# Kernel optimization log

Hardware: AMD Instinct MI355X
Metric: run time of the kernel (lower is better)

The kernel has to match this reference:

```python
import jax, jax.numpy as jnp
import numpy as np

NUM_EMBEDDINGS = 8192
EMBEDDING_DIM = 256
COMMITMENT_COST = 0.25


def setup_inputs() -> dict:
    key = jax.random.key(0)
    k1, k2 = jax.random.split(key)
    z_e = jax.random.normal(k1, (16, 2048, EMBEDDING_DIM), dtype=jnp.float32)
    # nn.Embedding init: uniform(-1/K, 1/K)
    codebook = jax.random.uniform(
        k2, (NUM_EMBEDDINGS, EMBEDDING_DIM), dtype=jnp.float32,
        minval=-1.0 / NUM_EMBEDDINGS, maxval=1.0 / NUM_EMBEDDINGS)
    return {"z_e": z_e, "codebook": codebook}


def _nearest_indices(z_flat, codebook):
    # squared euclidean distances; argmin is identical to argmin of cdist
    # z_flat: [T, D], codebook: [K, D] -> dist2: [T, K]
    x2 = jnp.sum(z_flat * z_flat, axis=-1, keepdims=True)          # [T, 1]
    w2 = jnp.sum(codebook * codebook, axis=-1)                      # [K]
    xw = jnp.einsum('td,kd->tk', z_flat, codebook)                  # [T, K]
    dist2 = x2 - 2.0 * xw + w2
    return jnp.argmin(dist2, axis=1)                                # [T]


def reference(z_e, codebook):
    original_shape = z_e.shape
    z_e_flat = z_e.reshape(-1, EMBEDDING_DIM)
    indices = _nearest_indices(z_e_flat, codebook)
    z_q = codebook[indices].reshape(original_shape)
    # straight-through estimator
    z_q_ste = z_e + jax.lax.stop_gradient(z_q - z_e)
    commitment_loss = jnp.mean((z_e - jax.lax.stop_gradient(z_q_ste)) ** 2)
    codebook_loss = jnp.mean((z_q_ste - jax.lax.stop_gradient(z_e)) ** 2)
    loss = codebook_loss + COMMITMENT_COST * commitment_loss
    # codebook usage: fraction of unique indices (jit-friendly via scatter)
    used = jnp.zeros((NUM_EMBEDDINGS,), dtype=jnp.float32).at[indices].set(1.0)
    usage = jnp.sum(used) / NUM_EMBEDDINGS
    return (z_q_ste, loss, usage)
```

## Files before the change

kernel.cpp:

```cpp
#include <hip/hip_runtime.h>
#include <float.h>

#define T_TOTAL 32768
#define KC      8192
#define DIM     256

#define LOSS_IDX  ((size_t)T_TOTAL * DIM)
#define USAGE_IDX (LOSS_IDX + 1)

typedef short s16x8 __attribute__((ext_vector_type(8)));
typedef float f32x4 __attribute__((ext_vector_type(4)));

#define WS_W2    0
#define WS_FLAGS 32768
#define WS_CBF   65536

__device__ __forceinline__ unsigned short f2bf(float f) {
    unsigned int u = __float_as_uint(f);
    u += 0x7FFFu + ((u >> 16) & 1u);
    return (unsigned short)(u >> 16);
}

__global__ __launch_bounds__(256) void vq_prep(const float* __restrict__ cb,
                                               unsigned short* __restrict__ cbb,
                                               float* __restrict__ w2,
                                               int* __restrict__ flags,
                                               float* __restrict__ out) {
    const int blk = blockIdx.x, tid = threadIdx.x;
    size_t i = (size_t)blk * 2048 + (size_t)tid * 8;
    float4 a = *(const float4*)(cb + i);
    float4 b = *(const float4*)(cb + i + 4);
    uint4 o;
    o.x = (unsigned)f2bf(a.x) | ((unsigned)f2bf(a.y) << 16);
    o.y = (unsigned)f2bf(a.z) | ((unsigned)f2bf(a.w) << 16);
    o.z = (unsigned)f2bf(b.x) | ((unsigned)f2bf(b.y) << 16);
    o.w = (unsigned)f2bf(b.z) | ((unsigned)f2bf(b.w) << 16);
    *(uint4*)(cbb + i) = o;
    float s = a.x * a.x + a.y * a.y + a.z * a.z + a.w * a.w
            + b.x * b.x + b.y * b.y + b.z * b.z + b.w * b.w;
    #pragma unroll
    for (int m = 1; m <= 16; m <<= 1) s += __shfl_xor(s, m);
    if ((tid & 31) == 0) w2[blk * 8 + (tid >> 5)] = s;
    if (blk < 32) flags[blk * 256 + tid] = 0;
    if (blk < 128) {
        int t = blk * 256 + tid;
        *(unsigned long long*)(out + ((size_t)t << 8)) = ~0ULL;
    }
    if (blk == 0 && tid == 0) { out[LOSS_IDX] = 0.0f; out[USAGE_IDX] = 0.0f; }
}

__global__ __launch_bounds__(512, 2) void vq_main(const unsigned short* __restrict__ cbb,
                                                  const float* __restrict__ w2g,
                                                  const float* __restrict__ z_e,
                                                  float* __restrict__ out) {
    __shared__ unsigned short ca[8][4][2048];

    const int tid  = threadIdx.x;
    const int lane = tid & 63;
    const int w    = tid >> 6;
    const int quad = lane >> 4;
    const int l15  = lane & 15;
    const int tb   = blockIdx.x >> 2;
    const int cq   = blockIdx.x & 3;
    const int t0   = tb * 512;
    const int cbase = cq * 2048;

    const int srow = lane >> 3;
    const int ssl  = lane & 7;
    const unsigned short* pstage = cbb + (size_t)(cbase + srow) * DIM + (ssl ^ srow) * 8;

    #define STAGE(PC, KW, BP)                                                           \
        {                                                                               \
            _Pragma("unroll")                                                           \
            for (int q = 0; q < 4; ++q) {                                               \
                __builtin_amdgcn_global_load_lds(                                       \
                    (const __attribute__((address_space(1))) void*)((PC) + (KW) * 64 + q * 2048), \
                    (__attribute__((address_space(3))) void*)(&ca[w][BP][q * 512]),     \
                    16, 0, 0);                                                          \
            }                                                                           \
        }

    const unsigned short* fragp[4];
    #pragma unroll
    for (int kk = 0; kk < 2; ++kk)
        #pragma unroll
        for (int j = 0; j < 2; ++j) {
            int row = j * 16 + l15;
            int sl = (kk * 4 + quad) ^ (l15 & 7);
            fragp[kk * 2 + j] = &ca[w][0][row * 64 + sl * 8];
        }

    #define READFRAGS(FB, BP)                                                           \
        {                                                                               \
            _Pragma("unroll")                                                           \
            for (int f = 0; f < 4; ++f)                                                 \
                (FB)[f] = *(const s16x8*)(fragp[f] + (BP) * 2048);                      \
        }

    STAGE(pstage, 0, 0); STAGE(pstage, 1, 1); STAGE(pstage, 2, 2); STAGE(pstage, 3, 3);
    s16x8 af[4][8];
    #pragma unroll
    for (int i = 0; i < 4; ++i) {
        #pragma unroll
        for (int ks = 0; ks < 8; ++ks) {
            const float* p = z_e + (size_t)(t0 + w * 64 + i * 16 + l15) * DIM + ks * 32 + quad * 8;
            float4 a = *(const float4*)p;
            float4 b = *(const float4*)(p + 4);
            s16x8 v;
            v[0] = (short)f2bf(a.x); v[1] = (short)f2bf(a.y);
            v[2] = (short)f2bf(a.z); v[3] = (short)f2bf(a.w);
            v[4] = (short)f2bf(b.x); v[5] = (short)f2bf(b.y);
            v[6] = (short)f2bf(b.z); v[7] = (short)f2bf(b.w);
            af[i][ks] = v;
        }
    }

    float best[4][4];
    int   bidx[4][4];
    #pragma unroll
    for (int i = 0; i < 4; ++i)
        #pragma unroll
        for (int r = 0; r < 4; ++r) { best[i][r] = FLT_MAX; bidx[i][r] = 0x7FFFFFFF; }

    const float* pw2 = w2g + cbase + l15;

    s16x8 regB[2][4];
    __builtin_amdgcn_s_waitcnt(0x0F7C);
    READFRAGS(regB[0], 0);

    for (int c = 0; c < 64; ++c) {
        f32x4 acc[4][2];
        #pragma unroll
        for (int i = 0; i < 4; ++i)
            #pragma unroll
            for (int j = 0; j < 2; ++j) acc[i][j] = (f32x4){0.f, 0.f, 0.f, 0.f};

        const unsigned short* pcn = pstage + ((size_t)((c + 1) & 63) << 13);

        #pragma unroll
        for (int kw = 0; kw < 4; ++kw) {
            __builtin_amdgcn_s_waitcnt(0xC07F);
            STAGE(pcn, kw, kw);
            __builtin_amdgcn_s_waitcnt(0x0F78);
            READFRAGS(regB[(kw + 1) & 1], (kw + 1) & 3);
            const s16x8* cur = regB[kw & 1];
            __builtin_amdgcn_s_setprio(1);
            #pragma unroll
            for (int kk = 0; kk < 2; ++kk)
                #pragma unroll
                for (int i = 0; i < 4; ++i)
                    #pragma unroll
                    for (int j = 0; j < 2; ++j)
                        acc[i][j] = __builtin_amdgcn_mfma_f32_16x16x32_bf16(af[i][kw * 2 + kk], cur[kk * 2 + j], acc[i][j], 0, 0, 0);
            __builtin_amdgcn_s_setprio(0);
        }

        #pragma unroll
        for (int j = 0; j < 2; ++j) {
            int col = cbase + c * 32 + j * 16 + l15;
            float w2v = pw2[c * 32 + j * 16];
            #pragma unroll
            for (int i = 0; i < 4; ++i)
                #pragma unroll
                for (int r = 0; r < 4; ++r) {
                    float s = fmaf(-2.0f, acc[i][j][r], w2v);
                    if (s < best[i][r]) { best[i][r] = s; bidx[i][r] = col; }
                }
        }
    }

    #pragma unroll
    for (int i = 0; i < 4; ++i)
        #pragma unroll
        for (int r = 0; r < 4; ++r) {
            float b = best[i][r]; int ix = bidx[i][r];
            #pragma unroll
            for (int m = 1; m < 16; m <<= 1) {
                float ob = __shfl_xor(b, m);
                int   oi = __shfl_xor(ix, m);
                if (ob < b || (ob == b && oi < ix)) { b = ob; ix = oi; }
            }
            if (l15 == 0) {
                unsigned int fb = __float_as_uint(b);
                fb = (fb & 0x80000000u) ? ~fb : (fb | 0x80000000u);
                unsigned long long key = ((unsigned long long)fb << 32) | (unsigned int)ix;
                int tok = t0 + w * 64 + i * 16 + quad * 4 + r;
                atomicMin((unsigned long long*)(out + ((size_t)tok << 8)), key);
            }
        }
}

__global__ __launch_bounds__(256) void vq_gather(const float* __restrict__ cb,
                                                 const float* __restrict__ z_e,
                                                 float* __restrict__ out,
                                                 int* __restrict__ flags) {
    __shared__ float wls[4];
    const int tid  = threadIdx.x;
    const int lane = tid & 63;
    const int w    = tid >> 6;
    const int t0   = blockIdx.x * 128;

    float lsum = 0.0f;
    for (int t = w * 32; t < w * 32 + 32; ++t) {
        int tok = t0 + t;
        unsigned long long key = *(const unsigned long long*)(out + ((size_t)tok << 8));
        int k = (int)(unsigned int)(key & 0xFFFFFFFFull);
        if (lane == 0) flags[k] = 1;
        float4 cv = *(const float4*)(cb + (size_t)k * DIM + lane * 4);
        float4 zv = *(const float4*)(z_e + (size_t)tok * DIM + lane * 4);
        float dx = zv.x - cv.x, dy = zv.y - cv.y, dz = zv.z - cv.z, dw = zv.w - cv.w;
        lsum += dx * dx + dy * dy + dz * dz + dw * dw;
        *(float4*)(out + ((size_t)tok << 8) + lane * 4) = cv;
    }
    #pragma unroll
    for (int m = 32; m >= 1; m >>= 1) lsum += __shfl_xor(lsum, m);
    if (lane == 0) wls[w] = lsum;
    __syncthreads();
    if (tid == 0) {
        float bsum = wls[0] + wls[1] + wls[2] + wls[3];
        atomicAdd(out + LOSS_IDX, bsum * (1.25f / (float)LOSS_IDX));
    }
}

__global__ __launch_bounds__(256) void vq_usage(const int* __restrict__ flags,
                                                float* __restrict__ out) {
    __shared__ int ws[4];
    int tid = threadIdx.x;
    int s = 0;
    for (int i = tid; i < KC; i += 256) s += flags[i];
    #pragma unroll
    for (int m = 32; m >= 1; m >>= 1) s += __shfl_xor(s, m);
    if ((tid & 63) == 0) ws[tid >> 6] = s;
    __syncthreads();
    if (tid == 0) out[USAGE_IDX] = (float)(ws[0] + ws[1] + ws[2] + ws[3]) / (float)KC;
}

extern "C" void kernel_launch(void* const* d_in, const int* in_sizes, int n_in,
                              void* d_out, int out_size, void* d_ws, size_t ws_size,
                              hipStream_t stream) {
    (void)in_sizes; (void)n_in; (void)out_size; (void)ws_size;
    const float* z_e = (const float*)d_in[0];
    const float* cb  = (const float*)d_in[1];
    float* out = (float*)d_out;

    char* ws = (char*)d_ws;
    float* w2    = (float*)(ws + WS_W2);
    int*   flags = (int*)(ws + WS_FLAGS);
    unsigned short* cbb = (unsigned short*)(ws + WS_CBF);

    vq_prep<<<KC / 8, 256, 0, stream>>>(cb, cbb, w2, flags, out);
    vq_main<<<256, 512, 0, stream>>>(cbb, w2, z_e, out);
    vq_gather<<<T_TOTAL / 128, 256, 0, stream>>>(cb, z_e, out, flags);
    vq_usage<<<1, 256, 0, stream>>>(flags, out);
}
```

Before: 261.0 us.

## Load codebook fragments directly to registers, fold usage count into gather

The main kernel drops the LDS staging of the bf16 codebook through global_load_lds and instead loads each wave's B fragments straight from global memory into registers, prefetching one k-step ahead. The squared norms are staged into shared memory once per block. The separate usage kernel is removed: the gather kernel counts first-time codebook hits with atomicExch plus atomicAdd, and it now runs twice as many blocks with fewer tokens each. This saves LDS traffic and one launch. In exchange, every wave issues redundant global/L2 reads of the codebook with no swizzled reuse, and more atomics land on a single float.

```diff
diff --git a/kernel.cpp b/kernel.cpp
--- a/kernel.cpp
+++ b/kernel.cpp
@@ -53,7 +53,7 @@
                                                   const float* __restrict__ w2g,
                                                   const float* __restrict__ z_e,
                                                   float* __restrict__ out) {
-    __shared__ unsigned short ca[8][4][2048];
+    __shared__ float w2s[2048];
 
     const int tid  = threadIdx.x;
     const int lane = tid & 63;
@@ -65,39 +65,10 @@
     const int t0   = tb * 512;
     const int cbase = cq * 2048;
 
-    const int srow = lane >> 3;
-    const int ssl  = lane & 7;
-    const unsigned short* pstage = cbb + (size_t)(cbase + srow) * DIM + (ssl ^ srow) * 8;
-
-    #define STAGE(PC, KW, BP)                                                           \
-        {                                                                               \
-            _Pragma("unroll")                                                           \
-            for (int q = 0; q < 4; ++q) {                                               \
-                __builtin_amdgcn_global_load_lds(                                       \
-                    (const __attribute__((address_space(1))) void*)((PC) + (KW) * 64 + q * 2048), \
-                    (__attribute__((address_space(3))) void*)(&ca[w][BP][q * 512]),     \
-                    16, 0, 0);                                                          \
-            }                                                                           \
-        }
-
-    const unsigned short* fragp[4];
-    #pragma unroll
-    for (int kk = 0; kk < 2; ++kk)
-        #pragma unroll
-        for (int j = 0; j < 2; ++j) {
-            int row = j * 16 + l15;
-            int sl = (kk * 4 + quad) ^ (l15 & 7);
-            fragp[kk * 2 + j] = &ca[w][0][row * 64 + sl * 8];
-        }
-
-    #define READFRAGS(FB, BP)                                                           \
-        {                                                                               \
-            _Pragma("unroll")                                                           \
-            for (int f = 0; f < 4; ++f)                                                 \
-                (FB)[f] = *(const s16x8*)(fragp[f] + (BP) * 2048);                      \
-        }
-
-    STAGE(pstage, 0, 0); STAGE(pstage, 1, 1); STAGE(pstage, 2, 2); STAGE(pstage, 3, 3);
+    const unsigned short* pb0 = cbb + (size_t)(cbase + l15) * DIM + quad * 8;
+    const unsigned short* pb1 = pb0 + 16 * DIM;
+
+    ((float4*)w2s)[tid] = ((const float4*)(w2g + cbase))[tid];
     s16x8 af[4][8];
     #pragma unroll
     for (int i = 0; i < 4; ++i) {
@@ -122,11 +93,13 @@
         #pragma unroll
         for (int r = 0; r < 4; ++r) { best[i][r] = FLT_MAX; bidx[i][r] = 0x7FFFFFFF; }
 
-    const float* pw2 = w2g + cbase + l15;
+    __syncthreads();
 
     s16x8 regB[2][4];
-    __builtin_amdgcn_s_waitcnt(0x0F7C);
-    READFRAGS(regB[0], 0);
+    regB[0][0] = *(const s16x8*)(pb0);
+    regB[0][1] = *(const s16x8*)(pb1);
+    regB[0][2] = *(const s16x8*)(pb0 + 32);
+    regB[0][3] = *(const s16x8*)(pb1 + 32);
 
     for (int c = 0; c < 64; ++c) {
         f32x4 acc[4][2];
@@ -135,14 +108,16 @@
             #pragma unroll
             for (int j = 0; j < 2; ++j) acc[i][j] = (f32x4){0.f, 0.f, 0.f, 0.f};
 
-        const unsigned short* pcn = pstage + ((size_t)((c + 1) & 63) << 13);
-
         #pragma unroll
         for (int kw = 0; kw < 4; ++kw) {
-            __builtin_amdgcn_s_waitcnt(0xC07F);
-            STAGE(pcn, kw, kw);
-            __builtin_amdgcn_s_waitcnt(0x0F78);
-            READFRAGS(regB[(kw + 1) & 1], (kw + 1) & 3);
+            const int c2  = (kw < 3) ? c : ((c + 1) & 63);
+            const int kw2 = (kw + 1) & 3;
+            const unsigned short* q0 = pb0 + (size_t)c2 * 8192;
+            const unsigned short* q1 = pb1 + (size_t)c2 * 8192;
+            s16x8 nf0 = *(const s16x8*)(q0 + kw2 * 64);
+            s16x8 nf1 = *(const s16x8*)(q1 + kw2 * 64);
+            s16x8 nf2 = *(const s16x8*)(q0 + kw2 * 64 + 32);
+            s16x8 nf3 = *(const s16x8*)(q1 + kw2 * 64 + 32);
             const s16x8* cur = regB[kw & 1];
             __builtin_amdgcn_s_setprio(1);
             #pragma unroll
@@ -153,12 +128,16 @@
                     for (int j = 0; j < 2; ++j)
                         acc[i][j] = __builtin_amdgcn_mfma_f32_16x16x32_bf16(af[i][kw * 2 + kk], cur[kk * 2 + j], acc[i][j], 0, 0, 0);
             __builtin_amdgcn_s_setprio(0);
+            regB[(kw + 1) & 1][0] = nf0;
+            regB[(kw + 1) & 1][1] = nf1;
+            regB[(kw + 1) & 1][2] = nf2;
+            regB[(kw + 1) & 1][3] = nf3;
         }
 
         #pragma unroll
         for (int j = 0; j < 2; ++j) {
             int col = cbase + c * 32 + j * 16 + l15;
-            float w2v = pw2[c * 32 + j * 16];
+            float w2v = w2s[c * 32 + j * 16 + l15];
             #pragma unroll
             for (int i = 0; i < 4; ++i)
                 #pragma unroll
@@ -198,14 +177,17 @@
     const int tid  = threadIdx.x;
     const int lane = tid & 63;
     const int w    = tid >> 6;
-    const int t0   = blockIdx.x * 128;
+    const int t0   = blockIdx.x * 64;
 
     float lsum = 0.0f;
-    for (int t = w * 32; t < w * 32 + 32; ++t) {
+    for (int t = w * 16; t < w * 16 + 16; ++t) {
         int tok = t0 + t;
         unsigned long long key = *(const unsigned long long*)(out + ((size_t)tok << 8));
         int k = (int)(unsigned int)(key & 0xFFFFFFFFull);
-        if (lane == 0) flags[k] = 1;
+        if (lane == 0) {
+            if (atomicExch(&flags[k], 1) == 0)
+                atomicAdd(out + USAGE_IDX, 1.0f / (float)KC);
+        }
         float4 cv = *(const float4*)(cb + (size_t)k * DIM + lane * 4);
         float4 zv = *(const float4*)(z_e + (size_t)tok * DIM + lane * 4);
         float dx = zv.x - cv.x, dy = zv.y - cv.y, dz = zv.z - cv.z, dw = zv.w - cv.w;
@@ -220,19 +202,6 @@
         float bsum = wls[0] + wls[1] + wls[2] + wls[3];
         atomicAdd(out + LOSS_IDX, bsum * (1.25f / (float)LOSS_IDX));
     }
-}
-
-__global__ __launch_bounds__(256) void vq_usage(const int* __restrict__ flags,
-                                                float* __restrict__ out) {
-    __shared__ int ws[4];
-    int tid = threadIdx.x;
-    int s = 0;
-    for (int i = tid; i < KC; i += 256) s += flags[i];
-    #pragma unroll
-    for (int m = 32; m >= 1; m >>= 1) s += __shfl_xor(s, m);
-    if ((tid & 63) == 0) ws[tid >> 6] = s;
-    __syncthreads();
-    if (tid == 0) out[USAGE_IDX] = (float)(ws[0] + ws[1] + ws[2] + ws[3]) / (float)KC;
 }
 
 extern "C" void kernel_launch(void* const* d_in, const int* in_sizes, int n_in,
@@ -250,6 +219,5 @@
 
     vq_prep<<<KC / 8, 256, 0, stream>>>(cb, cbb, w2, flags, out);
     vq_main<<<256, 512, 0, stream>>>(cbb, w2, z_e, out);
-    vq_gather<<<T_TOTAL / 128, 256, 0, stream>>>(cb, z_e, out, flags);
-    vq_usage<<<1, 256, 0, stream>>>(flags, out);
-}
+    vq_gather<<<T_TOTAL / 64, 256, 0, stream>>>(cb, z_e, out, flags);
+}
```

Result: slower. 455.2 us (+74.4%).

## Share codebook LDS tiles across warps and prefetch gather indices

Applied to the files above, without the earlier changes.

In the main kernel, each wave used to stage its own private copy of the same codebook chunk into LDS. Now one block-wide buffer is filled by a rotating subset of waves, with barriers and waitcnts to synchronise it. This cuts redundant global-to-LDS traffic and LDS footprint, which may allow more occupancy. The w2 norms are also staged once into LDS instead of read from global each chunk. The gather kernel loads 16 indices per wave up front, broadcasts them with shuffles, and launches more blocks with shorter loops. The cost is a block barrier on every k-step, which may serialise waves in the MFMA loop.

```diff
diff --git a/kernel.cpp b/kernel.cpp
--- a/kernel.cpp
+++ b/kernel.cpp
@@ -53,7 +53,8 @@
                                                   const float* __restrict__ w2g,
                                                   const float* __restrict__ z_e,
                                                   float* __restrict__ out) {
-    __shared__ unsigned short ca[8][4][2048];
+    __shared__ unsigned short cs[4 * 2048];
+    __shared__ float w2s[2048];
 
     const int tid  = threadIdx.x;
     const int lane = tid & 63;
@@ -69,13 +70,13 @@
     const int ssl  = lane & 7;
     const unsigned short* pstage = cbb + (size_t)(cbase + srow) * DIM + (ssl ^ srow) * 8;
 
-    #define STAGE(PC, KW, BP)                                                           \
+    #define STAGEW(PC, KW)                                                              \
         {                                                                               \
             _Pragma("unroll")                                                           \
             for (int q = 0; q < 4; ++q) {                                               \
                 __builtin_amdgcn_global_load_lds(                                       \
                     (const __attribute__((address_space(1))) void*)((PC) + (KW) * 64 + q * 2048), \
-                    (__attribute__((address_space(3))) void*)(&ca[w][BP][q * 512]),     \
+                    (__attribute__((address_space(3))) void*)(&cs[(KW) * 2048 + q * 512]), \
                     16, 0, 0);                                                          \
             }                                                                           \
         }
@@ -87,7 +88,7 @@
         for (int j = 0; j < 2; ++j) {
             int row = j * 16 + l15;
             int sl = (kk * 4 + quad) ^ (l15 & 7);
-            fragp[kk * 2 + j] = &ca[w][0][row * 64 + sl * 8];
+            fragp[kk * 2 + j] = &cs[row * 64 + sl * 8];
         }
 
     #define READFRAGS(FB, BP)                                                           \
@@ -97,7 +98,8 @@
                 (FB)[f] = *(const s16x8*)(fragp[f] + (BP) * 2048);                      \
         }
 
-    STAGE(pstage, 0, 0); STAGE(pstage, 1, 1); STAGE(pstage, 2, 2); STAGE(pstage, 3, 3);
+    ((float4*)w2s)[tid] = ((const float4*)(w2g + cbase))[tid];
+    if (w < 4) STAGEW(pstage, w);
     s16x8 af[4][8];
     #pragma unroll
     for (int i = 0; i < 4; ++i) {
@@ -122,26 +124,28 @@
         #pragma unroll
         for (int r = 0; r < 4; ++r) { best[i][r] = FLT_MAX; bidx[i][r] = 0x7FFFFFFF; }
 
-    const float* pw2 = w2g + cbase + l15;
-
     s16x8 regB[2][4];
-    __builtin_amdgcn_s_waitcnt(0x0F7C);
+    __builtin_amdgcn_s_waitcnt(0x0F70);
+    __syncthreads();
     READFRAGS(regB[0], 0);
+    __builtin_amdgcn_s_waitcnt(0xC07F);
+    __builtin_amdgcn_s_barrier();
 
     for (int c = 0; c < 64; ++c) {
+        const int sb = (c & 1) ? 0 : 4;
+        const int db = (c & 1) ? 6 : 2;
+        const unsigned short* pcn = pstage + ((size_t)((c + 1) & 63) << 13);
+
         f32x4 acc[4][2];
         #pragma unroll
         for (int i = 0; i < 4; ++i)
             #pragma unroll
             for (int j = 0; j < 2; ++j) acc[i][j] = (f32x4){0.f, 0.f, 0.f, 0.f};
 
-        const unsigned short* pcn = pstage + ((size_t)((c + 1) & 63) << 13);
-
         #pragma unroll
         for (int kw = 0; kw < 4; ++kw) {
-            __builtin_amdgcn_s_waitcnt(0xC07F);
-            STAGE(pcn, kw, kw);
-            __builtin_amdgcn_s_waitcnt(0x0F78);
+            if (w == sb + kw) STAGEW(pcn, kw);
+            if (w == ((db + kw) & 7)) __builtin_amdgcn_s_waitcnt(0x0F70);
             READFRAGS(regB[(kw + 1) & 1], (kw + 1) & 3);
             const s16x8* cur = regB[kw & 1];
             __builtin_amdgcn_s_setprio(1);
@@ -153,12 +157,14 @@
                     for (int j = 0; j < 2; ++j)
                         acc[i][j] = __builtin_amdgcn_mfma_f32_16x16x32_bf16(af[i][kw * 2 + kk], cur[kk * 2 + j], acc[i][j], 0, 0, 0);
             __builtin_amdgcn_s_setprio(0);
+            __builtin_amdgcn_s_waitcnt(0xC07F);
+            __builtin_amdgcn_s_barrier();
         }
 
         #pragma unroll
         for (int j = 0; j < 2; ++j) {
             int col = cbase + c * 32 + j * 16 + l15;
-            float w2v = pw2[c * 32 + j * 16];
+            float w2v = w2s[c * 32 + j * 16 + l15];
             #pragma unroll
             for (int i = 0; i < 4; ++i)
                 #pragma unroll
@@ -198,13 +204,17 @@
     const int tid  = threadIdx.x;
     const int lane = tid & 63;
     const int w    = tid >> 6;
-    const int t0   = blockIdx.x * 128;
+    const int tw   = blockIdx.x * 64 + w * 16;
+
+    int myk = 0;
+    if (lane < 16)
+        myk = (int)(unsigned int)(*(const unsigned long long*)(out + ((size_t)(tw + lane) << 8)) & 0xFFFFFFFFull);
 
     float lsum = 0.0f;
-    for (int t = w * 32; t < w * 32 + 32; ++t) {
-        int tok = t0 + t;
-        unsigned long long key = *(const unsigned long long*)(out + ((size_t)tok << 8));
-        int k = (int)(unsigned int)(key & 0xFFFFFFFFull);
+    #pragma unroll 4
+    for (int i = 0; i < 16; ++i) {
+        int tok = tw + i;
+        int k = __shfl(myk, i);
         if (lane == 0) flags[k] = 1;
         float4 cv = *(const float4*)(cb + (size_t)k * DIM + lane * 4);
         float4 zv = *(const float4*)(z_e + (size_t)tok * DIM + lane * 4);
@@ -250,6 +260,6 @@
 
     vq_prep<<<KC / 8, 256, 0, stream>>>(cb, cbb, w2, flags, out);
     vq_main<<<256, 512, 0, stream>>>(cbb, w2, z_e, out);
-    vq_gather<<<T_TOTAL / 128, 256, 0, stream>>>(cb, z_e, out, flags);
+    vq_gather<<<T_TOTAL / 64, 256, 0, stream>>>(cb, z_e, out, flags);
     vq_usage<<<1, 256, 0, stream>>>(flags, out);
 }
```

New measurement: 255.6 us. 2.0% less time.

## Fuse codebook gather and loss into main kernel via per-token-block barrier

Applied to the files above, without the earlier changes.

Folds the separate gather/loss kernel into the end of the main argmin kernel. The four blocks that share a token tile synchronize through a global counter with a spin-wait, then each gathers a quarter of the tokens, writes the quantized rows, sets usage flags and accumulates the loss. This removes one kernel launch and the associated global round-trip. It also stages the codebook norms in shared memory instead of reading them from global each chunk. The spin barrier relies on all 256 blocks being co-resident (2 per CU by launch bounds); otherwise it could deadlock, and the added LDS could lower occupancy.

```diff
diff --git a/kernel.cpp b/kernel.cpp
--- a/kernel.cpp
+++ b/kernel.cpp
@@ -13,7 +13,8 @@
 
 #define WS_W2    0
 #define WS_FLAGS 32768
-#define WS_CBF   65536
+#define WS_GCNT  65536
+#define WS_CBF   65792
 
 __device__ __forceinline__ unsigned short f2bf(float f) {
     unsigned int u = __float_as_uint(f);
@@ -25,6 +26,7 @@
                                                unsigned short* __restrict__ cbb,
                                                float* __restrict__ w2,
                                                int* __restrict__ flags,
+                                               int* __restrict__ gcnt,
                                                float* __restrict__ out) {
     const int blk = blockIdx.x, tid = threadIdx.x;
     size_t i = (size_t)blk * 2048 + (size_t)tid * 8;
@@ -42,6 +44,7 @@
     for (int m = 1; m <= 16; m <<= 1) s += __shfl_xor(s, m);
     if ((tid & 31) == 0) w2[blk * 8 + (tid >> 5)] = s;
     if (blk < 32) flags[blk * 256 + tid] = 0;
+    if (blk == 0 && tid < 64) gcnt[tid] = 0;
     if (blk < 128) {
         int t = blk * 256 + tid;
         *(unsigned long long*)(out + ((size_t)t << 8)) = ~0ULL;
@@ -52,8 +55,13 @@
 __global__ __launch_bounds__(512, 2) void vq_main(const unsigned short* __restrict__ cbb,
                                                   const float* __restrict__ w2g,
                                                   const float* __restrict__ z_e,
-                                                  float* __restrict__ out) {
+                                                  const float* __restrict__ cb,
+                                                  float* __restrict__ out,
+                                                  int* __restrict__ flags,
+                                                  int* __restrict__ gcnt) {
     __shared__ unsigned short ca[8][4][2048];
+    __shared__ float w2s[2048];
+    __shared__ float wls[8];
 
     const int tid  = threadIdx.x;
     const int lane = tid & 63;
@@ -97,6 +105,7 @@
                 (FB)[f] = *(const s16x8*)(fragp[f] + (BP) * 2048);                      \
         }
 
+    ((float4*)w2s)[tid] = ((const float4*)(w2g + cbase))[tid];
     STAGE(pstage, 0, 0); STAGE(pstage, 1, 1); STAGE(pstage, 2, 2); STAGE(pstage, 3, 3);
     s16x8 af[4][8];
     #pragma unroll
@@ -122,10 +131,9 @@
         #pragma unroll
         for (int r = 0; r < 4; ++r) { best[i][r] = FLT_MAX; bidx[i][r] = 0x7FFFFFFF; }
 
-    const float* pw2 = w2g + cbase + l15;
-
     s16x8 regB[2][4];
-    __builtin_amdgcn_s_waitcnt(0x0F7C);
+    __builtin_amdgcn_s_waitcnt(0x0F70);
+    __syncthreads();
     READFRAGS(regB[0], 0);
 
     for (int c = 0; c < 64; ++c) {
@@ -158,7 +166,7 @@
         #pragma unroll
         for (int j = 0; j < 2; ++j) {
             int col = cbase + c * 32 + j * 16 + l15;
-            float w2v = pw2[c * 32 + j * 16];
+            float w2v = w2s[c * 32 + j * 16 + l15];
             #pragma unroll
             for (int i = 0; i < 4; ++i)
                 #pragma unroll
@@ -188,23 +196,26 @@
                 atomicMin((unsigned long long*)(out + ((size_t)tok << 8)), key);
             }
         }
-}
-
-__global__ __launch_bounds__(256) void vq_gather(const float* __restrict__ cb,
-                                                 const float* __restrict__ z_e,
-                                                 float* __restrict__ out,
-                                                 int* __restrict__ flags) {
-    __shared__ float wls[4];
-    const int tid  = threadIdx.x;
-    const int lane = tid & 63;
-    const int w    = tid >> 6;
-    const int t0   = blockIdx.x * 128;
+
+    __threadfence();
+    __syncthreads();
+    if (tid == 0) {
+        atomicAdd(&gcnt[tb], 1);
+        while (atomicAdd(&gcnt[tb], 0) < 4) __builtin_amdgcn_s_sleep(2);
+    }
+    __syncthreads();
+
+    const int gbase = t0 + cq * 128 + w * 16;
+    unsigned long long mykey = 0;
+    if (lane < 16)
+        mykey = atomicMin((unsigned long long*)(out + ((size_t)(gbase + lane) << 8)), ~0ULL);
+    int myk = (int)(unsigned int)(mykey & 0xFFFFFFFFull);
 
     float lsum = 0.0f;
-    for (int t = w * 32; t < w * 32 + 32; ++t) {
-        int tok = t0 + t;
-        unsigned long long key = *(const unsigned long long*)(out + ((size_t)tok << 8));
-        int k = (int)(unsigned int)(key & 0xFFFFFFFFull);
+    #pragma unroll 4
+    for (int i = 0; i < 16; ++i) {
+        int tok = gbase + i;
+        int k = __shfl(myk, i);
         if (lane == 0) flags[k] = 1;
         float4 cv = *(const float4*)(cb + (size_t)k * DIM + lane * 4);
         float4 zv = *(const float4*)(z_e + (size_t)tok * DIM + lane * 4);
@@ -217,7 +228,9 @@
     if (lane == 0) wls[w] = lsum;
     __syncthreads();
     if (tid == 0) {
-        float bsum = wls[0] + wls[1] + wls[2] + wls[3];
+        float bsum = 0.0f;
+        #pragma unroll
+        for (int q = 0; q < 8; ++q) bsum += wls[q];
         atomicAdd(out + LOSS_IDX, bsum * (1.25f / (float)LOSS_IDX));
     }
 }
@@ -246,10 +259,10 @@
     char* ws = (char*)d_ws;
     float* w2    = (float*)(ws + WS_W2);
     int*   flags = (int*)(ws + WS_FLAGS);
+    int*   gcnt  = (int*)(ws + WS_GCNT);
     unsigned short* cbb = (unsigned short*)(ws + WS_CBF);
 
-    vq_prep<<<KC / 8, 256, 0, stream>>>(cb, cbb, w2, flags, out);
-    vq_main<<<256, 512, 0, stream>>>(cbb, w2, z_e, out);
-    vq_gather<<<T_TOTAL / 128, 256, 0, stream>>>(cb, z_e, out, flags);
+    vq_prep<<<KC / 8, 256, 0, stream>>>(cb, cbb, w2, flags, gcnt, out);
+    vq_main<<<256, 512, 0, stream>>>(cbb, w2, z_e, cb, out, flags, gcnt);
     vq_usage<<<1, 256, 0, stream>>>(flags, out);
 }
```

Result: slower. 269.9 us (+3.4%).
